# Optimization experiments

Hardware: AMD Instinct MI355X
Metric: run time of the kernel (lower is better)

Reference implementation:

```python
import jax, jax.numpy as jnp
import numpy as np

HID = 1024   # hidden_size
NH = 16      # num_heads
HD = HID // NH   # 64 head_dim
RD = int(HD * 0.25)  # 16 rotary_dim
B = 2
S = 2048
ROPE_BASE = 10000.0


def setup_inputs() -> dict:
    key = jax.random.key(0)
    ks = jax.random.split(key, 4)
    hidden_states = jax.random.normal(ks[0], (B, S, HID), jnp.float32)
    # torch nn.Linear weights: [out_features, in_features]
    Wqkv = jax.random.normal(ks[1], (3 * HID, HID), jnp.float32) * (HID ** -0.5)
    bqkv = jnp.zeros((3 * HID,), jnp.float32)
    Wd = jax.random.normal(ks[2], (HID, HID), jnp.float32) * (HID ** -0.5)
    bd = jnp.zeros((HID,), jnp.float32)
    return {"hidden_states": hidden_states, "Wqkv": Wqkv, "bqkv": bqkv, "Wd": Wd, "bd": bd}


def _rotary_tables(seq_len):
    inv_freq = 1.0 / (ROPE_BASE ** (jnp.arange(0, RD, 2, dtype=jnp.float32) / RD))
    t = jnp.arange(seq_len, dtype=jnp.float32)
    freqs = jnp.outer(t, inv_freq)                       # [S, RD/2]
    emb = jnp.concatenate([freqs, freqs], axis=-1)       # [S, RD]
    return jnp.cos(emb)[None, None], jnp.sin(emb)[None, None]  # [1,1,S,RD]


def _rotate_half(x):
    x1, x2 = jnp.split(x, 2, axis=-1)
    return jnp.concatenate([-x2, x1], axis=-1)


def reference(hidden_states, Wqkv, bqkv, Wd, bd):
    b, s, _ = hidden_states.shape
    qkv = hidden_states @ Wqkv.T + bqkv                  # [b,s,3*HID]
    qkv = qkv.reshape(b, s, 3, NH, HD).transpose(2, 0, 3, 1, 4)  # [3,b,nh,s,hd]
    q, k, v = qkv[0], qkv[1], qkv[2]

    cos, sin = _rotary_tables(s)
    q_rot, q_pass = q[..., :RD], q[..., RD:]
    k_rot, k_pass = k[..., :RD], k[..., RD:]
    q_rot = q_rot * cos + _rotate_half(q_rot) * sin
    k_rot = k_rot * cos + _rotate_half(k_rot) * sin
    q = jnp.concatenate([q_rot, q_pass], axis=-1)
    k = jnp.concatenate([k_rot, k_pass], axis=-1)

    scale = HD ** -0.5
    logits = jnp.einsum('bhqd,bhkd->bhqk', q, k) * scale  # [b,nh,s,s]
    causal_mask = jnp.triu(jnp.full((s, s), -jnp.inf, dtype=logits.dtype), 1)
    probs = jax.nn.softmax(logits + causal_mask, axis=-1)

    # KA recurrence: A_i = p_ii * V_i + sum_{j<i} p_ij * A_j
    # <=> (I - strict_lower(P)) A = diag(P) * V  -> batched triangular solve
    L = jnp.eye(s, dtype=probs.dtype) - jnp.tril(probs, -1)      # [b,nh,s,s]
    rhs = jnp.diagonal(probs, axis1=-2, axis2=-1)[..., None] * v  # [b,nh,s,hd]
    A = jax.scipy.linalg.solve_triangular(L, rhs, lower=True)     # [b,nh,s,hd]

    attn_output = A.transpose(0, 2, 1, 3).reshape(b, s, HID)
    return attn_output @ Wd.T + bd
```

## Files before the change

### kernel.cpp

```cpp
#include <hip/hip_runtime.h>
#include <math.h>

namespace {

constexpr int B  = 2, S = 2048, NH = 16, HD = 64, HID = 1024;
constexpr int BH = B * NH;
constexpr int NSTEP2 = 8;

constexpr size_t OFF_A    = 4194304;
constexpr size_t OFF_Q    = 12582912;
constexpr size_t OFF_K    = 16777216;
constexpr size_t OFF_V    = 20971520;
constexpr size_t OFF_ZI   = 25231360;
constexpr size_t OFF_PD   = 25296896;
constexpr size_t OFF_UP   = 25362432;
constexpr size_t WS_FLOATS = 29294592;

typedef __attribute__((ext_vector_type(8))) short bf16x8;
typedef __attribute__((ext_vector_type(4))) float f32x4;

__device__ inline unsigned short bf_rne(float x) {
  const unsigned u = __float_as_uint(x);
  return (unsigned short)((u + 0x7FFFu + ((u >> 16) & 1u)) >> 16);
}
__device__ inline float bf2f(short h) {
  return __uint_as_float((unsigned)(unsigned short)h << 16);
}
__device__ inline void split8(const float4 a, const float4 b,
                              bf16x8& hi, bf16x8& lo) {
  float v[8] = {a.x, a.y, a.z, a.w, b.x, b.y, b.z, b.w};
#pragma unroll
  for (int i = 0; i < 8; ++i) {
    const unsigned short h = bf_rne(v[i]);
    hi[i] = (short)h;
    lo[i] = (short)bf_rne(v[i] - bf2f((short)h));
  }
}
__device__ inline f32x4 apply3(const short* __restrict__ mh_,
                               const short* __restrict__ ml_,
                               const float* __restrict__ brow, int lg) {
  f32x4 o = (f32x4)0.f;
#pragma unroll
  for (int ks = 0; ks < 2; ++ks) {
    const bf16x8 mh = *(const bf16x8*)(mh_ + ks * 32 + lg * 8);
    const bf16x8 ml = *(const bf16x8*)(ml_ + ks * 32 + lg * 8);
    const float* bp = brow + ks * 32 + lg * 8;
    bf16x8 bh, bl;
    split8(*(const float4*)bp, *(const float4*)(bp + 4), bh, bl);
    o = __builtin_amdgcn_mfma_f32_16x16x32_bf16(mh, bh, o, 0, 0, 0);
    o = __builtin_amdgcn_mfma_f32_16x16x32_bf16(ml, bh, o, 0, 0, 0);
    o = __builtin_amdgcn_mfma_f32_16x16x32_bf16(mh, bl, o, 0, 0, 0);
  }
  return o;
}

__global__ __launch_bounds__(256) void split_pre(
    const float* __restrict__ hs, short* __restrict__ h1, short* __restrict__ l1,
    const float* __restrict__ wq, short* __restrict__ h2, short* __restrict__ l2) {
  const int n1 = B * S * HID / 4;
  const int n2 = 3 * HID * HID / 4;
  for (int g = blockIdx.x * 256 + threadIdx.x; g < n1 + n2; g += gridDim.x * 256) {
    const bool first = g < n1;
    const int idx = first ? g : g - n1;
    const float4 x = first ? *(const float4*)(hs + (size_t)idx * 4)
                           : *(const float4*)(wq + (size_t)idx * 4);
    short4 h, l;
    h.x = bf_rne(x.x); h.y = bf_rne(x.y); h.z = bf_rne(x.z); h.w = bf_rne(x.w);
    l.x = bf_rne(x.x - bf2f(h.x));
    l.y = bf_rne(x.y - bf2f(h.y));
    l.z = bf_rne(x.z - bf2f(h.z));
    l.w = bf_rne(x.w - bf2f(h.w));
    if (first) {
      *(short4*)(h1 + (size_t)idx * 4) = h;
      *(short4*)(l1 + (size_t)idx * 4) = l;
    } else {
      *(short4*)(h2 + (size_t)idx * 4) = h;
      *(short4*)(l2 + (size_t)idx * 4) = l;
    }
  }
}

__global__ __launch_bounds__(256) void split_post(
    const float* __restrict__ Abuf, short* __restrict__ h1, short* __restrict__ l1,
    const float* __restrict__ wd, short* __restrict__ h2, short* __restrict__ l2) {
  const int n1 = B * S * HID / 4;
  const int n2 = HID * HID / 4;
  for (int g = blockIdx.x * 256 + threadIdx.x; g < n1 + n2; g += gridDim.x * 256) {
    float4 x;
    if (g < n1) {
      const int m = g >> 8, q = g & 255;
      const int k0 = q * 4;
      const int b = m >> 11, s = m & (S - 1);
      const int h = k0 >> 6, d = k0 & 63;
      x = *(const float4*)(Abuf + (((size_t)(b * NH + h) * S + s) << 6) + d);
    } else {
      x = *(const float4*)(wd + (size_t)(g - n1) * 4);
    }
    short4 h, l;
    h.x = bf_rne(x.x); h.y = bf_rne(x.y); h.z = bf_rne(x.z); h.w = bf_rne(x.w);
    l.x = bf_rne(x.x - bf2f(h.x));
    l.y = bf_rne(x.y - bf2f(h.y));
    l.z = bf_rne(x.z - bf2f(h.z));
    l.w = bf_rne(x.w - bf2f(h.w));
    if (g < n1) {
      *(short4*)(h1 + (size_t)g * 4) = h;
      *(short4*)(l1 + (size_t)g * 4) = l;
    } else {
      *(short4*)(h2 + (size_t)(g - n1) * 4) = h;
      *(short4*)(l2 + (size_t)(g - n1) * 4) = l;
    }
  }
}

__global__ __launch_bounds__(256) void gemm_bf3(
    const short* __restrict__ Ahi, const short* __restrict__ Alo,
    const short* __restrict__ Bhi, const short* __restrict__ Blo,
    const float* __restrict__ bias, float* __restrict__ C,
    int M, int N, int K) {
  __shared__ short ash[128][40], als[128][40], bsh[128][40], bls[128][40];
  const int t = threadIdx.x;
  const int m0 = blockIdx.y * 128, n0 = blockIdx.x * 128;
  const int w = t >> 6, l = t & 63;
  const int wm = (w >> 1) * 64, wn = (w & 1) * 64;
  const int lr = l & 15, lk = (l >> 4) * 8;
  f32x4 acc[4][4];
#pragma unroll
  for (int i = 0; i < 4; ++i)
#pragma unroll
    for (int j = 0; j < 4; ++j) acc[i][j] = (f32x4)0.f;

  for (int kb = 0; kb < K; kb += 32) {
    __syncthreads();
#pragma unroll
    for (int i = 0; i < 2; ++i) {
      const int idx = t + i * 256;
      const int row = idx >> 2, c8 = (idx & 3) * 8;
      *(uint4*)&ash[row][c8] = *(const uint4*)(Ahi + (size_t)(m0 + row) * K + kb + c8);
      *(uint4*)&als[row][c8] = *(const uint4*)(Alo + (size_t)(m0 + row) * K + kb + c8);
      *(uint4*)&bsh[row][c8] = *(const uint4*)(Bhi + (size_t)(n0 + row) * K + kb + c8);
      *(uint4*)&bls[row][c8] = *(const uint4*)(Blo + (size_t)(n0 + row) * K + kb + c8);
    }
    __syncthreads();
    bf16x8 ah[4], al[4], bh[4], bl[4];
#pragma unroll
    for (int mi = 0; mi < 4; ++mi) {
      ah[mi] = *(const bf16x8*)&ash[wm + mi * 16 + lr][lk];
      al[mi] = *(const bf16x8*)&als[wm + mi * 16 + lr][lk];
    }
#pragma unroll
    for (int ni = 0; ni < 4; ++ni) {
      bh[ni] = *(const bf16x8*)&bsh[wn + ni * 16 + lr][lk];
      bl[ni] = *(const bf16x8*)&bls[wn + ni * 16 + lr][lk];
    }
#pragma unroll
    for (int mi = 0; mi < 4; ++mi)
#pragma unroll
      for (int ni = 0; ni < 4; ++ni) {
        acc[mi][ni] = __builtin_amdgcn_mfma_f32_16x16x32_bf16(
            ah[mi], bh[ni], acc[mi][ni], 0, 0, 0);
        acc[mi][ni] = __builtin_amdgcn_mfma_f32_16x16x32_bf16(
            al[mi], bh[ni], acc[mi][ni], 0, 0, 0);
        acc[mi][ni] = __builtin_amdgcn_mfma_f32_16x16x32_bf16(
            ah[mi], bl[ni], acc[mi][ni], 0, 0, 0);
      }
  }
  const int rq = (l >> 4) * 4;
#pragma unroll
  for (int ni = 0; ni < 4; ++ni) {
    const int col = n0 + wn + ni * 16 + lr;
    const float bv = bias[col];
#pragma unroll
    for (int mi = 0; mi < 4; ++mi)
#pragma unroll
      for (int r = 0; r < 4; ++r) {
        const int row = m0 + wm + mi * 16 + rq + r;
        C[(size_t)row * N + col] = acc[mi][ni][r] + bv;
      }
  }
}

__global__ __launch_bounds__(256) void k2_rope(
    const float* __restrict__ qkv, short* __restrict__ Qhi,
    short* __restrict__ Qlo, short* __restrict__ Khi,
    short* __restrict__ Klo, float* __restrict__ V) {
  const int g  = blockIdx.x * 256 + threadIdx.x;
  const int s  = g & (S - 1);
  const int bh = g >> 11;
  const int b  = bh >> 4, h = bh & 15;
  const float* base = qkv + ((size_t)b * S + s) * 3072 + h * 64;
  float q[64], k[64], v[64];
#pragma unroll
  for (int f = 0; f < 16; ++f) {
    const float4 x = *(const float4*)(base + f * 4);
    q[f*4+0]=x.x; q[f*4+1]=x.y; q[f*4+2]=x.z; q[f*4+3]=x.w;
    const float4 y = *(const float4*)(base + 1024 + f * 4);
    k[f*4+0]=y.x; k[f*4+1]=y.y; k[f*4+2]=y.z; k[f*4+3]=y.w;
    const float4 z = *(const float4*)(base + 2048 + f * 4);
    v[f*4+0]=z.x; v[f*4+1]=z.y; v[f*4+2]=z.z; v[f*4+3]=z.w;
  }
  const float PW[8] = {1.0f, 3.1622776601683795f, 10.0f, 31.622776601683793f,
                       100.0f, 316.22776601683796f, 1000.0f, 3162.2776601683795f};
  float qr[16], kr[16];
#pragma unroll
  for (int d = 0; d < 16; ++d) {
    const int j = d & 7;
    const float invf = 1.0f / PW[j];
    const float fr = (float)s * invf;
    float sn, c;
    sincosf(fr, &sn, &c);
    const float rq = (d < 8) ? -q[d + 8] : q[d - 8];
    const float rk = (d < 8) ? -k[d + 8] : k[d - 8];
    qr[d] = q[d] * c + rq * sn;
    kr[d] = k[d] * c + rk * sn;
  }
#pragma unroll
  for (int d = 0; d < 16; ++d) { q[d] = qr[d]; k[d] = kr[d]; }
#pragma unroll
  for (int d = 0; d < 64; ++d) q[d] *= 0.125f;
  const size_t o = ((size_t)bh * S + s) << 6;
  float* vd = V + o;
#pragma unroll
  for (int f = 0; f < 16; ++f) {
    short4 qh, ql, kh, kl;
    const float* qq = q + f * 4;
    const float* kk = k + f * 4;
    qh.x = bf_rne(qq[0]); qh.y = bf_rne(qq[1]); qh.z = bf_rne(qq[2]); qh.w = bf_rne(qq[3]);
    ql.x = bf_rne(qq[0]-bf2f(qh.x)); ql.y = bf_rne(qq[1]-bf2f(qh.y));
    ql.z = bf_rne(qq[2]-bf2f(qh.z)); ql.w = bf_rne(qq[3]-bf2f(qh.w));
    kh.x = bf_rne(kk[0]); kh.y = bf_rne(kk[1]); kh.z = bf_rne(kk[2]); kh.w = bf_rne(kk[3]);
    kl.x = bf_rne(kk[0]-bf2f(kh.x)); kl.y = bf_rne(kk[1]-bf2f(kh.y));
    kl.z = bf_rne(kk[2]-bf2f(kh.z)); kl.w = bf_rne(kk[3]-bf2f(kh.w));
    *(short4*)(Qhi + o + f*4) = qh;
    *(short4*)(Qlo + o + f*4) = ql;
    *(short4*)(Khi + o + f*4) = kh;
    *(short4*)(Klo + o + f*4) = kl;
    *(float4*)(vd + f*4) = make_float4(v[f*4], v[f*4+1], v[f*4+2], v[f*4+3]);
  }
}

__global__ __launch_bounds__(256) void k3_scores(
    const short* __restrict__ Qhi, const short* __restrict__ Qlo,
    const short* __restrict__ Khi, const short* __restrict__ Klo,
    float* __restrict__ partZ, float* __restrict__ sdg) {
  const int cb = blockIdx.x, rb = blockIdx.y, bh = blockIdx.z;
  if (cb > rb) return;
  __shared__ short qh[128][72], ql[128][72], kh[128][72], kl[128][72];
  __shared__ float red[128][2];
  const int t = threadIdx.x;
  const int w = t >> 6, l = t & 63;
  const int wm = (w >> 1) * 64, wn = (w & 1) * 64;
  const int lr = l & 15, lg = l >> 4;
  for (int v = t; v < 1024; v += 256) {
    const int r = v >> 3, c8 = (v & 7) * 8;
    const size_t gq = (((size_t)bh * S + rb * 128 + r) << 6) + c8;
    const size_t gk = (((size_t)bh * S + cb * 128 + r) << 6) + c8;
    *(uint4*)&qh[r][c8] = *(const uint4*)(Qhi + gq);
    *(uint4*)&ql[r][c8] = *(const uint4*)(Qlo + gq);
    *(uint4*)&kh[r][c8] = *(const uint4*)(Khi + gk);
    *(uint4*)&kl[r][c8] = *(const uint4*)(Klo + gk);
  }
  __syncthreads();
  f32x4 acc[4][4];
#pragma unroll
  for (int i = 0; i < 4; ++i)
#pragma unroll
    for (int j = 0; j < 4; ++j) acc[i][j] = (f32x4)0.f;
#pragma unroll
  for (int ks = 0; ks < 2; ++ks) {
    const int lk = ks * 32 + lg * 8;
    bf16x8 ah[4], al[4], bhf[4], blf[4];
#pragma unroll
    for (int mi = 0; mi < 4; ++mi) {
      ah[mi] = *(const bf16x8*)&qh[wm + mi * 16 + lr][lk];
      al[mi] = *(const bf16x8*)&ql[wm + mi * 16 + lr][lk];
    }
#pragma unroll
    for (int ni = 0; ni < 4; ++ni) {
      bhf[ni] = *(const bf16x8*)&kh[wn + ni * 16 + lr][lk];
      blf[ni] = *(const bf16x8*)&kl[wn + ni * 16 + lr][lk];
    }
#pragma unroll
    for (int mi = 0; mi < 4; ++mi)
#pragma unroll
      for (int ni = 0; ni < 4; ++ni) {
        acc[mi][ni] = __builtin_amdgcn_mfma_f32_16x16x32_bf16(
            ah[mi], bhf[ni], acc[mi][ni], 0, 0, 0);
        acc[mi][ni] = __builtin_amdgcn_mfma_f32_16x16x32_bf16(
            al[mi], bhf[ni], acc[mi][ni], 0, 0, 0);
        acc[mi][ni] = __builtin_amdgcn_mfma_f32_16x16x32_bf16(
            ah[mi], blf[ni], acc[mi][ni], 0, 0, 0);
      }
  }
  const int rq = lg * 4;
  const int rowbase = rb * 128 + wm, colbase = cb * 128 + wn;
  float rp[4][4];
#pragma unroll
  for (int mi = 0; mi < 4; ++mi)
#pragma unroll
    for (int r = 0; r < 4; ++r) rp[mi][r] = 0.f;
#pragma unroll
  for (int mi = 0; mi < 4; ++mi)
#pragma unroll
    for (int ni = 0; ni < 4; ++ni)
#pragma unroll
      for (int r = 0; r < 4; ++r) {
        const int rG = rowbase + mi * 16 + rq + r;
        const int cG = colbase + ni * 16 + lr;
        if (cG <= rG) rp[mi][r] += __expf(acc[mi][ni][r]);
        if (cG == rG) sdg[(size_t)bh * S + rG] = acc[mi][ni][r];
      }
#pragma unroll
  for (int off = 1; off < 16; off <<= 1)
#pragma unroll
    for (int mi = 0; mi < 4; ++mi)
#pragma unroll
      for (int r = 0; r < 4; ++r)
        rp[mi][r] += __shfl_xor(rp[mi][r], off, 64);
  if (lr == 0)
#pragma unroll
    for (int mi = 0; mi < 4; ++mi)
#pragma unroll
      for (int r = 0; r < 4; ++r)
        red[wm + mi * 16 + rq + r][w & 1] = rp[mi][r];
  __syncthreads();
  if (t < 128)
    partZ[(((size_t)bh * 16 + rb) * 16 + cb) * 128 + t] = red[t][0] + red[t][1];
}

__global__ __launch_bounds__(256) void k3_reduce(
    const float* __restrict__ partZ, float* __restrict__ zinv,
    float* __restrict__ pdg) {
  const int R = blockIdx.x * 256 + threadIdx.x;
  const int bh = R >> 11, r = R & 2047;
  const int rb = r >> 7, row = r & 127;
  float Z = 0.f;
  for (int c = 0; c <= rb; ++c)
    Z += partZ[(((size_t)bh*16 + rb)*16 + c)*128 + row];
  const float zi = 1.f / Z;
  zinv[R] = zi;
  pdg[R] = __expf(pdg[R]) * zi;
}

__global__ __launch_bounds__(256) void k4_minv(
    const short* __restrict__ Qhi, const short* __restrict__ Qlo,
    const short* __restrict__ Khi, const short* __restrict__ Klo,
    const float* __restrict__ zinv, short* __restrict__ Mrh,
    short* __restrict__ Mrl, short* __restrict__ P10h,
    short* __restrict__ P10l) {
  const int bh = blockIdx.y, ib = blockIdx.x;
  const int r0 = ib * 64;
  __shared__ float Nb[64][68];
  __shared__ float X[64][68];
  const int t = threadIdx.x;
  const int w = t >> 6, l = t & 63;
  const int lr = l & 15, lg = l >> 4;

  bf16x8 qfh[2], qfl[2];
  const size_t qbase = (((size_t)bh * S + r0 + 16 * w + lr) << 6);
#pragma unroll
  for (int ks = 0; ks < 2; ++ks) {
    qfh[ks] = *(const bf16x8*)(Qhi + qbase + ks * 32 + lg * 8);
    qfl[ks] = *(const bf16x8*)(Qlo + qbase + ks * 32 + lg * 8);
  }
  const int rloc0 = 16 * w + lg * 4;
  float ziv[4];
#pragma unroll
  for (int i = 0; i < 4; ++i) ziv[i] = zinv[(size_t)bh * S + r0 + rloc0 + i];

  {
    f32x4 acc[4];
#pragma unroll
    for (int i = 0; i < 4; ++i) acc[i] = (f32x4)0.f;
    const size_t kbase = ((size_t)bh * S + r0) << 6;
#pragma unroll
    for (int ks = 0; ks < 2; ++ks) {
#pragma unroll
      for (int ni = 0; ni < 4; ++ni) {
        const size_t kb = kbase + (((size_t)(16 * ni + lr)) << 6) + ks * 32 + lg * 8;
        const bf16x8 bhf = *(const bf16x8*)(Khi + kb);
        const bf16x8 blf = *(const bf16x8*)(Klo + kb);
        acc[ni] = __builtin_amdgcn_mfma_f32_16x16x32_bf16(qfh[ks], bhf, acc[ni], 0, 0, 0);
        acc[ni] = __builtin_amdgcn_mfma_f32_16x16x32_bf16(qfl[ks], bhf, acc[ni], 0, 0, 0);
        acc[ni] = __builtin_amdgcn_mfma_f32_16x16x32_bf16(qfh[ks], blf, acc[ni], 0, 0, 0);
      }
    }
#pragma unroll
    for (int ni = 0; ni < 4; ++ni) {
      const int c = 16 * ni + lr;
#pragma unroll
      for (int i = 0; i < 4; ++i) {
        const int r = rloc0 + i;
        Nb[r][c] = (c < r) ? __expf(acc[ni][i]) * ziv[i] : 0.f;
      }
    }
  }
  if (ib & 1) {
    f32x4 p[4];
#pragma unroll
    for (int i = 0; i < 4; ++i) p[i] = (f32x4)0.f;
    const size_t kbase = ((size_t)bh * S + r0 - 64) << 6;
#pragma unroll
    for (int ks = 0; ks < 2; ++ks) {
#pragma unroll
      for (int ni = 0; ni < 4; ++ni) {
        const size_t kb = kbase + (((size_t)(16 * ni + lr)) << 6) + ks * 32 + lg * 8;
        const bf16x8 bhf = *(const bf16x8*)(Khi + kb);
        const bf16x8 blf = *(const bf16x8*)(Klo + kb);
        p[ni] = __builtin_amdgcn_mfma_f32_16x16x32_bf16(qfh[ks], bhf, p[ni], 0, 0, 0);
        p[ni] = __builtin_amdgcn_mfma_f32_16x16x32_bf16(qfl[ks], bhf, p[ni], 0, 0, 0);
        p[ni] = __builtin_amdgcn_mfma_f32_16x16x32_bf16(qfh[ks], blf, p[ni], 0, 0, 0);
      }
    }
    const size_t pbase = (((size_t)bh * 16 + (ib >> 1)) * 64) * 64;
#pragma unroll
    for (int ni = 0; ni < 4; ++ni) {
      const int c = 16 * ni + lr;
#pragma unroll
      for (int i = 0; i < 4; ++i) {
        const float val = __expf(p[ni][i]) * ziv[i];
        const unsigned short h = bf_rne(val);
        P10h[pbase + (size_t)(rloc0 + i) * 64 + c] = (short)h;
        P10l[pbase + (size_t)(rloc0 + i) * 64 + c] = (short)bf_rne(val - bf2f((short)h));
      }
    }
  }
  {
    const int c = t & 63, g = t >> 6;
#pragma unroll
    for (int i = 0; i < 16; ++i) {
      const int r = 16 * g + i;
      X[r][c] = (r == c) ? 1.f : 0.f;
    }
  }
  __syncthreads();

  const int c = t & 63, g = t >> 6;
  if (w == 0) {
    for (int rr = 1; rr < 16; ++rr) {
      float a = 0.f;
      for (int j = 0; j < rr; ++j) a += Nb[rr][j] * X[j][l];
      X[rr][l] += a;
    }
  }
  __syncthreads();
#pragma unroll
  for (int I = 1; I < 4; ++I) {
    {
      const int rb4 = 16 * I + 4 * g;
      float s0 = 0.f, s1 = 0.f, s2 = 0.f, s3 = 0.f;
      for (int j = 0; j < 16 * I; j += 4) {
        const float4 n0 = *(const float4*)&Nb[rb4 + 0][j];
        const float4 n1 = *(const float4*)&Nb[rb4 + 1][j];
        const float4 n2 = *(const float4*)&Nb[rb4 + 2][j];
        const float4 n3 = *(const float4*)&Nb[rb4 + 3][j];
        const float x0 = X[j + 0][c], x1 = X[j + 1][c];
        const float x2 = X[j + 2][c], x3 = X[j + 3][c];
        s0 += n0.x * x0 + n0.y * x1 + n0.z * x2 + n0.w * x3;
        s1 += n1.x * x0 + n1.y * x1 + n1.z * x2 + n1.w * x3;
        s2 += n2.x * x0 + n2.y * x1 + n2.z * x2 + n2.w * x3;
        s3 += n3.x * x0 + n3.y * x1 + n3.z * x2 + n3.w * x3;
      }
      X[rb4 + 0][c] += s0; X[rb4 + 1][c] += s1;
      X[rb4 + 2][c] += s2; X[rb4 + 3][c] += s3;
    }
    __syncthreads();
    if (w == 0) {
      const int rb = 16 * I;
      for (int rr = 1; rr < 16; ++rr) {
        const int r = rb + rr;
        float a = 0.f;
        for (int j = rb; j < r; ++j) a += Nb[r][j] * X[j][l];
        X[r][l] += a;
      }
    }
    __syncthreads();
  }

  const size_t mb = (((size_t)bh * 32 + ib) * 64) * 64;
  for (int v = t; v < 4096; v += 256) {
    const int r = v >> 6, cc = v & 63;
    const float x = X[r][cc];
    const unsigned short h = bf_rne(x);
    Mrh[mb + v] = (short)h;
    Mrl[mb + v] = (short)bf_rne(x - bf2f((short)h));
  }
}

__global__ __launch_bounds__(256) void k5_acc(
    const short* __restrict__ Qhi, const short* __restrict__ Qlo,
    const short* __restrict__ Khi, const short* __restrict__ Klo,
    const float* __restrict__ Abuf, const float* __restrict__ zinv,
    float* __restrict__ up, int s) {
  const int bh = blockIdx.z, rh = blockIdx.y, g = blockIdx.x;
  __shared__ float Es[128][68];
  __shared__ float Ats[64][68];
  const int t = threadIdx.x;
  const int w = t >> 6, l = t & 63;
  const int lr = l & 15, lg = l >> 4;
  const int rw = 32 * w;
  const int base = s * 256 + rh * 128;

  bf16x8 qfh[2][2], qfl[2][2];
#pragma unroll
  for (int mi = 0; mi < 2; ++mi)
#pragma unroll
    for (int ks = 0; ks < 2; ++ks) {
      const size_t qo = (((size_t)bh * S + base + rw + mi * 16 + lr) << 6) + ks * 32 + lg * 8;
      qfh[mi][ks] = *(const bf16x8*)(Qhi + qo);
      qfl[mi][ks] = *(const bf16x8*)(Qlo + qo);
    }
  float ziv[2][4];
#pragma unroll
  for (int mi = 0; mi < 2; ++mi)
#pragma unroll
    for (int r = 0; r < 4; ++r)
      ziv[mi][r] = zinv[(size_t)bh * S + base + rw + mi * 16 + lg * 4 + r];

  f32x4 out[2][4];
#pragma unroll
  for (int mi = 0; mi < 2; ++mi)
#pragma unroll
    for (int ni = 0; ni < 4; ++ni) out[mi][ni] = (f32x4)0.f;

  for (int j = g; j < 2 * s; j += 7) {
    for (int h = 0; h < 2; ++h) {
      __syncthreads();
      for (int v = t; v < 1024; v += 256) {
        const int d = v & 63, sq = v >> 6;
        const size_t ab = ((size_t)bh * S + j * 128 + h * 64 + sq * 4) << 6;
        float4 o;
        o.x = Abuf[ab + d];
        o.y = Abuf[ab + 64 + d];
        o.z = Abuf[ab + 128 + d];
        o.w = Abuf[ab + 192 + d];
        *(float4*)&Ats[d][sq * 4] = o;
      }
      f32x4 qk[2][4];
#pragma unroll
      for (int mi = 0; mi < 2; ++mi)
#pragma unroll
        for (int ni = 0; ni < 4; ++ni) qk[mi][ni] = (f32x4)0.f;
#pragma unroll
      for (int ks = 0; ks < 2; ++ks) {
#pragma unroll
        for (int ni = 0; ni < 4; ++ni) {
          const size_t ko = (((size_t)bh * S + j * 128 + h * 64 + ni * 16 + lr) << 6) + ks * 32 + lg * 8;
          const bf16x8 kh8 = *(const bf16x8*)(Khi + ko);
          const bf16x8 kl8 = *(const bf16x8*)(Klo + ko);
#pragma unroll
          for (int mi = 0; mi < 2; ++mi) {
            qk[mi][ni] = __builtin_amdgcn_mfma_f32_16x16x32_bf16(
                qfh[mi][ks], kh8, qk[mi][ni], 0, 0, 0);
            qk[mi][ni] = __builtin_amdgcn_mfma_f32_16x16x32_bf16(
                qfl[mi][ks], kh8, qk[mi][ni], 0, 0, 0);
            qk[mi][ni] = __builtin_amdgcn_mfma_f32_16x16x32_bf16(
                qfh[mi][ks], kl8, qk[mi][ni], 0, 0, 0);
          }
        }
      }
#pragma unroll
      for (int mi = 0; mi < 2; ++mi)
#pragma unroll
        for (int ni = 0; ni < 4; ++ni)
#pragma unroll
          for (int r = 0; r < 4; ++r)
            Es[rw + mi * 16 + lg * 4 + r][ni * 16 + lr] =
                __expf(qk[mi][ni][r]) * ziv[mi][r];
      __syncthreads();
#pragma unroll
      for (int ks = 0; ks < 2; ++ks) {
        bf16x8 eh[2], el[2];
#pragma unroll
        for (int mi = 0; mi < 2; ++mi) {
          const float* ep = &Es[rw + mi * 16 + lr][ks * 32 + lg * 8];
          split8(*(const float4*)ep, *(const float4*)(ep + 4), eh[mi], el[mi]);
        }
#pragma unroll
        for (int ni = 0; ni < 4; ++ni) {
          const float* ap = &Ats[ni * 16 + lr][ks * 32 + lg * 8];
          bf16x8 ah8, al8;
          split8(*(const float4*)ap, *(const float4*)(ap + 4), ah8, al8);
#pragma unroll
          for (int mi = 0; mi < 2; ++mi) {
            out[mi][ni] = __builtin_amdgcn_mfma_f32_16x16x32_bf16(
                eh[mi], ah8, out[mi][ni], 0, 0, 0);
            out[mi][ni] = __builtin_amdgcn_mfma_f32_16x16x32_bf16(
                el[mi], ah8, out[mi][ni], 0, 0, 0);
            out[mi][ni] = __builtin_amdgcn_mfma_f32_16x16x32_bf16(
                eh[mi], al8, out[mi][ni], 0, 0, 0);
          }
        }
      }
    }
  }
  float* ub = up + (((size_t)(bh * 7 + g) * 2 + rh) << 13);
#pragma unroll
  for (int mi = 0; mi < 2; ++mi)
#pragma unroll
    for (int ni = 0; ni < 4; ++ni)
#pragma unroll
      for (int r = 0; r < 4; ++r)
        ub[(size_t)(rw + mi * 16 + lg * 4 + r) * 64 + ni * 16 + lr] =
            out[mi][ni][r];
}

__global__ __launch_bounds__(256) void k5_fin(
    const short* __restrict__ Qhi, const short* __restrict__ Qlo,
    const short* __restrict__ Khi, const short* __restrict__ Klo,
    const float* __restrict__ V, const float* __restrict__ pd,
    const float* __restrict__ zinv, const float* __restrict__ up,
    const short* __restrict__ Mrh, const short* __restrict__ Mrl,
    const short* __restrict__ P10h, const short* __restrict__ P10l,
    float* __restrict__ Abuf, int s) {
  const int d0 = blockIdx.x * 16;
  const int bh = blockIdx.y;
  const int t = threadIdx.x;
  const int w = t >> 6, l = t & 63;
  const int lr = l & 15, lg = l >> 4;
  const int base = s * 256;
  __shared__ float uT[16][260];
  __shared__ float aT[16][132];
  __shared__ float Es[128][68];
  const int ng = (2 * s < 7) ? 2 * s : 7;

  for (int v = t; v < 1024; v += 256) {
    const int r = v >> 2, f = v & 3;
    const int R = base + r;
    const float4 x = *(const float4*)(V + (((size_t)bh * S + R) << 6) + d0 + f * 4);
    const float p = pd[(size_t)bh * S + R];
    float a0 = p * x.x, a1 = p * x.y, a2 = p * x.z, a3 = p * x.w;
    const int rh = r >> 7, rr = r & 127;
    for (int g = 0; g < ng; ++g) {
      const float4 y = *(const float4*)(
          up + (((size_t)(bh * 7 + g) * 2 + rh) << 13) + (rr << 6) + d0 + f * 4);
      a0 += y.x; a1 += y.y; a2 += y.z; a3 += y.w;
    }
    uT[f * 4 + 0][r] = a0; uT[f * 4 + 1][r] = a1;
    uT[f * 4 + 2][r] = a2; uT[f * 4 + 3][r] = a3;
  }
  __syncthreads();
  const size_t mstep = (size_t)bh * 32 + s * 4;
  {
    const size_t mb = ((mstep + 0) * 64 + 16 * w + lr) * 64;
    const f32x4 o = apply3(Mrh + mb, Mrl + mb, &uT[lr][0], lg);
#pragma unroll
    for (int i = 0; i < 4; ++i) {
      const int r = 16 * w + lg * 4 + i;
      Abuf[(((size_t)bh * S + base + r) << 6) + d0 + lr] = o[i];
      aT[lr][r] = o[i];
    }
  }
  __syncthreads();
  {
    const size_t pb = (((size_t)bh * 16 + 2 * s) * 64 + 16 * w + lr) * 64;
    const f32x4 o = apply3(P10h + pb, P10l + pb, &aT[lr][0], lg);
#pragma unroll
    for (int i = 0; i < 4; ++i)
      uT[lr][64 + 16 * w + lg * 4 + i] += o[i];
  }
  __syncthreads();
  {
    const size_t mb = ((mstep + 1) * 64 + 16 * w + lr) * 64;
    const f32x4 o = apply3(Mrh + mb, Mrl + mb, &uT[lr][64], lg);
#pragma unroll
    for (int i = 0; i < 4; ++i) {
      const int r = 16 * w + lg * 4 + i;
      Abuf[(((size_t)bh * S + base + 64 + r) << 6) + d0 + lr] = o[i];
      aT[lr][64 + r] = o[i];
    }
  }
  {
    const int rw = 32 * w;
    bf16x8 qh_[2][2], ql_[2][2];
#pragma unroll
    for (int mi = 0; mi < 2; ++mi)
#pragma unroll
      for (int ks = 0; ks < 2; ++ks) {
        const size_t qo = (((size_t)bh * S + base + 128 + rw + mi * 16 + lr) << 6) + ks * 32 + lg * 8;
        qh_[mi][ks] = *(const bf16x8*)(Qhi + qo);
        ql_[mi][ks] = *(const bf16x8*)(Qlo + qo);
      }
    float zv[2][4];
#pragma unroll
    for (int mi = 0; mi < 2; ++mi)
#pragma unroll
      for (int i = 0; i < 4; ++i)
        zv[mi][i] = zinv[(size_t)bh * S + base + 128 + rw + mi * 16 + lg * 4 + i];
    for (int ch = 0; ch < 2; ++ch) {
      __syncthreads();
      f32x4 qk[2][4];
#pragma unroll
      for (int mi = 0; mi < 2; ++mi)
#pragma unroll
        for (int ni = 0; ni < 4; ++ni) qk[mi][ni] = (f32x4)0.f;
#pragma unroll
      for (int ks = 0; ks < 2; ++ks) {
#pragma unroll
        for (int ni = 0; ni < 4; ++ni) {
          const size_t ko = (((size_t)bh * S + base + ch * 64 + ni * 16 + lr) << 6) + ks * 32 + lg * 8;
          const bf16x8 kh8 = *(const bf16x8*)(Khi + ko);
          const bf16x8 kl8 = *(const bf16x8*)(Klo + ko);
#pragma unroll
          for (int mi = 0; mi < 2; ++mi) {
            qk[mi][ni] = __builtin_amdgcn_mfma_f32_16x16x32_bf16(
                qh_[mi][ks], kh8, qk[mi][ni], 0, 0, 0);
            qk[mi][ni] = __builtin_amdgcn_mfma_f32_16x16x32_bf16(
                ql_[mi][ks], kh8, qk[mi][ni], 0, 0, 0);
            qk[mi][ni] = __builtin_amdgcn_mfma_f32_16x16x32_bf16(
                qh_[mi][ks], kl8, qk[mi][ni], 0, 0, 0);
          }
        }
      }
#pragma unroll
      for (int mi = 0; mi < 2; ++mi)
#pragma unroll
        for (int ni = 0; ni < 4; ++ni)
#pragma unroll
          for (int i = 0; i < 4; ++i)
            Es[rw + mi * 16 + lg * 4 + i][ni * 16 + lr] =
                __expf(qk[mi][ni][i]) * zv[mi][i];
      __syncthreads();
#pragma unroll
      for (int mi = 0; mi < 2; ++mi) {
        f32x4 o = (f32x4)0.f;
#pragma unroll
        for (int kq = 0; kq < 2; ++kq) {
          const float* ep = &Es[rw + mi * 16 + lr][kq * 32 + lg * 8];
          bf16x8 eh, el;
          split8(*(const float4*)ep, *(const float4*)(ep + 4), eh, el);
          const float* ap = &aT[lr][ch * 64 + kq * 32 + lg * 8];
          bf16x8 ah, al;
          split8(*(const float4*)ap, *(const float4*)(ap + 4), ah, al);
          o = __builtin_amdgcn_mfma_f32_16x16x32_bf16(eh, ah, o, 0, 0, 0);
          o = __builtin_amdgcn_mfma_f32_16x16x32_bf16(el, ah, o, 0, 0, 0);
          o = __builtin_amdgcn_mfma_f32_16x16x32_bf16(eh, al, o, 0, 0, 0);
        }
#pragma unroll
        for (int i = 0; i < 4; ++i)
          uT[lr][128 + rw + mi * 16 + lg * 4 + i] += o[i];
      }
    }
  }
  __syncthreads();
  {
    const size_t mb = ((mstep + 2) * 64 + 16 * w + lr) * 64;
    const f32x4 o = apply3(Mrh + mb, Mrl + mb, &uT[lr][128], lg);
#pragma unroll
    for (int i = 0; i < 4; ++i) {
      const int r = 16 * w + lg * 4 + i;
      Abuf[(((size_t)bh * S + base + 128 + r) << 6) + d0 + lr] = o[i];
      aT[lr][r] = o[i];
    }
  }
  __syncthreads();
  {
    const size_t pb = (((size_t)bh * 16 + 2 * s + 1) * 64 + 16 * w + lr) * 64;
    const f32x4 o = apply3(P10h + pb, P10l + pb, &aT[lr][0], lg);
#pragma unroll
    for (int i = 0; i < 4; ++i)
      uT[lr][192 + 16 * w + lg * 4 + i] += o[i];
  }
  __syncthreads();
  {
    const size_t mb = ((mstep + 3) * 64 + 16 * w + lr) * 64;
    const f32x4 o = apply3(Mrh + mb, Mrl + mb, &uT[lr][192], lg);
#pragma unroll
    for (int i = 0; i < 4; ++i) {
      const int r = 16 * w + lg * 4 + i;
      Abuf[(((size_t)bh * S + base + 192 + r) << 6) + d0 + lr] = o[i];
    }
  }
}

}

extern "C" void kernel_launch(void* const* d_in, const int* in_sizes, int n_in,
                              void* d_out, int out_size, void* d_ws, size_t ws_size,
                              hipStream_t stream) {
  const float* hs   = (const float*)d_in[0];
  const float* Wqkv = (const float*)d_in[1];
  const float* bqkv = (const float*)d_in[2];
  const float* Wd   = (const float*)d_in[3];
  const float* bd   = (const float*)d_in[4];
  float* out = (float*)d_out;
  float* W   = (float*)d_ws;
  if (ws_size < WS_FLOATS * sizeof(float)) return;

  float* qkv   = W;
  float* partZ = W;
  float* Abuf  = W + OFF_A;
  short* Qhi   = (short*)(W + OFF_Q);
  short* Qlo   = Qhi + 4194304;
  short* Khi   = (short*)(W + OFF_K);
  short* Klo   = Khi + 4194304;
  float* Vb    = W + OFF_V;
  float* zi    = W + OFF_ZI;
  float* pdg   = W + OFF_PD;
  float* up    = W + OFF_UP;

  char* wsb = (char*)d_ws;
  short* Ahi  = (short*)(wsb + 50331648);
  short* Alo  = Ahi + 4194304;
  short* Whi  = (short*)(wsb + 67108864);
  short* Wlo  = Whi + 3145728;
  short* A2hi = (short*)(wsb + 50331648);
  short* A2lo = A2hi + 4194304;
  short* Wdhi = (short*)(wsb + 67108864);
  short* Wdlo = Wdhi + 1048576;
  short* P10h = (short*)(wsb);
  short* P10l = P10h + 2097152;
  short* Mrh  = (short*)(wsb + 33554432);
  short* Mrl  = Mrh + 4194304;

  split_pre<<<dim3(2048), 256, 0, stream>>>(hs, Ahi, Alo, Wqkv, Whi, Wlo);
  gemm_bf3<<<dim3(24, 32), 256, 0, stream>>>(Ahi, Alo, Whi, Wlo, bqkv, qkv,
                                             B*S, 3*HID, HID);
  k2_rope<<<dim3(BH * S / 256), 256, 0, stream>>>(qkv, Qhi, Qlo, Khi, Klo, Vb);
  k3_scores<<<dim3(16, 16, BH), 256, 0, stream>>>(Qhi, Qlo, Khi, Klo, partZ, pdg);
  k3_reduce<<<dim3(BH * S / 256), 256, 0, stream>>>(partZ, zi, pdg);
  k4_minv<<<dim3(S / 64, BH), 256, 0, stream>>>(Qhi, Qlo, Khi, Klo, zi,
                                                Mrh, Mrl, P10h, P10l);
  for (int s = 0; s < NSTEP2; ++s) {
    if (s > 0) {
      const int ng = (2 * s < 7) ? 2 * s : 7;
      k5_acc<<<dim3(ng, 2, BH), 256, 0, stream>>>(Qhi, Qlo, Khi, Klo, Abuf, zi,
                                                  up, s);
    }
    k5_fin<<<dim3(4, BH), 256, 0, stream>>>(Qhi, Qlo, Khi, Klo, Vb, pdg, zi, up,
                                            Mrh, Mrl, P10h, P10l, Abuf, s);
  }
  split_post<<<dim3(2048), 256, 0, stream>>>(Abuf, A2hi, A2lo, Wd, Wdhi, Wdlo);
  gemm_bf3<<<dim3(8, 32), 256, 0, stream>>>(A2hi, A2lo, Wdhi, Wdlo, bd, out,
                                            B*S, HID, HID);
}
```

Baseline: 692.5 us.

## Fuse bf16 hi/lo splitting into GEMM loads and merge k5_acc row halves

Removes the split_pre and split_post kernels: the GEMM now loads fp32 inputs and splits them into bf16 hi/lo pairs while staging into shared memory, and the output GEMM gathers directly from the per-head A buffer. This avoids writing and re-reading the split bf16 copies. Separately, k5_acc now handles both 128-row halves in one block, so each A tile loaded into shared memory is reused for twice as many query rows. The cost is halving k5_acc's grid, which raises register pressure and lowers parallelism. The GEMM also repeats the split work on every tile load.

Result: slower. 782.0 us (+12.9%).

```diff
diff --git a/kernel.cpp b/kernel.cpp
--- a/kernel.cpp
+++ b/kernel.cpp
@@ -54,67 +54,9 @@
   return o;
 }
 
-__global__ __launch_bounds__(256) void split_pre(
-    const float* __restrict__ hs, short* __restrict__ h1, short* __restrict__ l1,
-    const float* __restrict__ wq, short* __restrict__ h2, short* __restrict__ l2) {
-  const int n1 = B * S * HID / 4;
-  const int n2 = 3 * HID * HID / 4;
-  for (int g = blockIdx.x * 256 + threadIdx.x; g < n1 + n2; g += gridDim.x * 256) {
-    const bool first = g < n1;
-    const int idx = first ? g : g - n1;
-    const float4 x = first ? *(const float4*)(hs + (size_t)idx * 4)
-                           : *(const float4*)(wq + (size_t)idx * 4);
-    short4 h, l;
-    h.x = bf_rne(x.x); h.y = bf_rne(x.y); h.z = bf_rne(x.z); h.w = bf_rne(x.w);
-    l.x = bf_rne(x.x - bf2f(h.x));
-    l.y = bf_rne(x.y - bf2f(h.y));
-    l.z = bf_rne(x.z - bf2f(h.z));
-    l.w = bf_rne(x.w - bf2f(h.w));
-    if (first) {
-      *(short4*)(h1 + (size_t)idx * 4) = h;
-      *(short4*)(l1 + (size_t)idx * 4) = l;
-    } else {
-      *(short4*)(h2 + (size_t)idx * 4) = h;
-      *(short4*)(l2 + (size_t)idx * 4) = l;
-    }
-  }
-}
-
-__global__ __launch_bounds__(256) void split_post(
-    const float* __restrict__ Abuf, short* __restrict__ h1, short* __restrict__ l1,
-    const float* __restrict__ wd, short* __restrict__ h2, short* __restrict__ l2) {
-  const int n1 = B * S * HID / 4;
-  const int n2 = HID * HID / 4;
-  for (int g = blockIdx.x * 256 + threadIdx.x; g < n1 + n2; g += gridDim.x * 256) {
-    float4 x;
-    if (g < n1) {
-      const int m = g >> 8, q = g & 255;
-      const int k0 = q * 4;
-      const int b = m >> 11, s = m & (S - 1);
-      const int h = k0 >> 6, d = k0 & 63;
-      x = *(const float4*)(Abuf + (((size_t)(b * NH + h) * S + s) << 6) + d);
-    } else {
-      x = *(const float4*)(wd + (size_t)(g - n1) * 4);
-    }
-    short4 h, l;
-    h.x = bf_rne(x.x); h.y = bf_rne(x.y); h.z = bf_rne(x.z); h.w = bf_rne(x.w);
-    l.x = bf_rne(x.x - bf2f(h.x));
-    l.y = bf_rne(x.y - bf2f(h.y));
-    l.z = bf_rne(x.z - bf2f(h.z));
-    l.w = bf_rne(x.w - bf2f(h.w));
-    if (g < n1) {
-      *(short4*)(h1 + (size_t)g * 4) = h;
-      *(short4*)(l1 + (size_t)g * 4) = l;
-    } else {
-      *(short4*)(h2 + (size_t)(g - n1) * 4) = h;
-      *(short4*)(l2 + (size_t)(g - n1) * 4) = l;
-    }
-  }
-}
-
-__global__ __launch_bounds__(256) void gemm_bf3(
-    const short* __restrict__ Ahi, const short* __restrict__ Alo,
-    const short* __restrict__ Bhi, const short* __restrict__ Blo,
+template<int GATHER>
+__global__ __launch_bounds__(256) void gemm_f32(
+    const float* __restrict__ A, const float* __restrict__ Bm,
     const float* __restrict__ bias, float* __restrict__ C,
     int M, int N, int K) {
   __shared__ short ash[128][40], als[128][40], bsh[128][40], bls[128][40];
@@ -135,10 +77,24 @@
     for (int i = 0; i < 2; ++i) {
       const int idx = t + i * 256;
       const int row = idx >> 2, c8 = (idx & 3) * 8;
-      *(uint4*)&ash[row][c8] = *(const uint4*)(Ahi + (size_t)(m0 + row) * K + kb + c8);
-      *(uint4*)&als[row][c8] = *(const uint4*)(Alo + (size_t)(m0 + row) * K + kb + c8);
-      *(uint4*)&bsh[row][c8] = *(const uint4*)(Bhi + (size_t)(n0 + row) * K + kb + c8);
-      *(uint4*)&bls[row][c8] = *(const uint4*)(Blo + (size_t)(n0 + row) * K + kb + c8);
+      const float* srcA;
+      if (GATHER) {
+        const int m = m0 + row;
+        const int b = m >> 11, ss = m & (S - 1);
+        const int kk = kb + c8;
+        const int h = kk >> 6, d = kk & 63;
+        srcA = A + (((size_t)(b * NH + h) * S + ss) << 6) + d;
+      } else {
+        srcA = A + (size_t)(m0 + row) * K + kb + c8;
+      }
+      bf16x8 hi, lo;
+      split8(*(const float4*)srcA, *(const float4*)(srcA + 4), hi, lo);
+      *(bf16x8*)&ash[row][c8] = hi;
+      *(bf16x8*)&als[row][c8] = lo;
+      const float* srcB = Bm + (size_t)(n0 + row) * K + kb + c8;
+      split8(*(const float4*)srcB, *(const float4*)(srcB + 4), hi, lo);
+      *(bf16x8*)&bsh[row][c8] = hi;
+      *(bf16x8*)&bls[row][c8] = lo;
     }
     __syncthreads();
     bf16x8 ah[4], al[4], bh[4], bl[4];
@@ -491,38 +447,46 @@
     const short* __restrict__ Khi, const short* __restrict__ Klo,
     const float* __restrict__ Abuf, const float* __restrict__ zinv,
     float* __restrict__ up, int s) {
-  const int bh = blockIdx.z, rh = blockIdx.y, g = blockIdx.x;
+  const int bh = blockIdx.y, g = blockIdx.x;
   __shared__ float Es[128][68];
   __shared__ float Ats[64][68];
   const int t = threadIdx.x;
   const int w = t >> 6, l = t & 63;
   const int lr = l & 15, lg = l >> 4;
   const int rw = 32 * w;
-  const int base = s * 256 + rh * 128;
-
-  bf16x8 qfh[2][2], qfl[2][2];
-#pragma unroll
-  for (int mi = 0; mi < 2; ++mi)
-#pragma unroll
-    for (int ks = 0; ks < 2; ++ks) {
-      const size_t qo = (((size_t)bh * S + base + rw + mi * 16 + lr) << 6) + ks * 32 + lg * 8;
-      qfh[mi][ks] = *(const bf16x8*)(Qhi + qo);
-      qfl[mi][ks] = *(const bf16x8*)(Qlo + qo);
-    }
-  float ziv[2][4];
-#pragma unroll
-  for (int mi = 0; mi < 2; ++mi)
-#pragma unroll
-    for (int r = 0; r < 4; ++r)
-      ziv[mi][r] = zinv[(size_t)bh * S + base + rw + mi * 16 + lg * 4 + r];
-
-  f32x4 out[2][4];
-#pragma unroll
-  for (int mi = 0; mi < 2; ++mi)
-#pragma unroll
-    for (int ni = 0; ni < 4; ++ni) out[mi][ni] = (f32x4)0.f;
-
-  for (int j = g; j < 2 * s; j += 7) {
+  const int base = s * 256;
+
+  bf16x8 qfh[2][2][2], qfl[2][2][2];
+#pragma unroll
+  for (int rh = 0; rh < 2; ++rh)
+#pragma unroll
+    for (int mi = 0; mi < 2; ++mi)
+#pragma unroll
+      for (int ks = 0; ks < 2; ++ks) {
+        const size_t qo = (((size_t)bh * S + base + rh * 128 + rw + mi * 16 + lr) << 6)
+                          + ks * 32 + lg * 8;
+        qfh[rh][mi][ks] = *(const bf16x8*)(Qhi + qo);
+        qfl[rh][mi][ks] = *(const bf16x8*)(Qlo + qo);
+      }
+  float ziv[2][2][4];
+#pragma unroll
+  for (int rh = 0; rh < 2; ++rh)
+#pragma unroll
+    for (int mi = 0; mi < 2; ++mi)
+#pragma unroll
+      for (int r = 0; r < 4; ++r)
+        ziv[rh][mi][r] =
+            zinv[(size_t)bh * S + base + rh * 128 + rw + mi * 16 + lg * 4 + r];
+
+  f32x4 out[2][2][4];
+#pragma unroll
+  for (int rh = 0; rh < 2; ++rh)
+#pragma unroll
+    for (int mi = 0; mi < 2; ++mi)
+#pragma unroll
+      for (int ni = 0; ni < 4; ++ni) out[rh][mi][ni] = (f32x4)0.f;
+
+  for (int j = g; j < 2 * s; j += gridDim.x) {
     for (int h = 0; h < 2; ++h) {
       __syncthreads();
       for (int v = t; v < 1024; v += 256) {
@@ -535,73 +499,80 @@
         o.w = Abuf[ab + 192 + d];
         *(float4*)&Ats[d][sq * 4] = o;
       }
-      f32x4 qk[2][4];
-#pragma unroll
-      for (int mi = 0; mi < 2; ++mi)
-#pragma unroll
-        for (int ni = 0; ni < 4; ++ni) qk[mi][ni] = (f32x4)0.f;
-#pragma unroll
-      for (int ks = 0; ks < 2; ++ks) {
-#pragma unroll
-        for (int ni = 0; ni < 4; ++ni) {
-          const size_t ko = (((size_t)bh * S + j * 128 + h * 64 + ni * 16 + lr) << 6) + ks * 32 + lg * 8;
-          const bf16x8 kh8 = *(const bf16x8*)(Khi + ko);
-          const bf16x8 kl8 = *(const bf16x8*)(Klo + ko);
-#pragma unroll
-          for (int mi = 0; mi < 2; ++mi) {
-            qk[mi][ni] = __builtin_amdgcn_mfma_f32_16x16x32_bf16(
-                qfh[mi][ks], kh8, qk[mi][ni], 0, 0, 0);
-            qk[mi][ni] = __builtin_amdgcn_mfma_f32_16x16x32_bf16(
-                qfl[mi][ks], kh8, qk[mi][ni], 0, 0, 0);
-            qk[mi][ni] = __builtin_amdgcn_mfma_f32_16x16x32_bf16(
-                qfh[mi][ks], kl8, qk[mi][ni], 0, 0, 0);
+      __syncthreads();
+#pragma unroll
+      for (int rh = 0; rh < 2; ++rh) {
+        f32x4 qk[2][4];
+#pragma unroll
+        for (int mi = 0; mi < 2; ++mi)
+#pragma unroll
+          for (int ni = 0; ni < 4; ++ni) qk[mi][ni] = (f32x4)0.f;
+#pragma unroll
+        for (int ks = 0; ks < 2; ++ks) {
+#pragma unroll
+          for (int ni = 0; ni < 4; ++ni) {
+            const size_t ko = (((size_t)bh * S + j * 128 + h * 64 + ni * 16 + lr) << 6)
+                              + ks * 32 + lg * 8;
+            const bf16x8 kh8 = *(const bf16x8*)(Khi + ko);
+            const bf16x8 kl8 = *(const bf16x8*)(Klo + ko);
+#pragma unroll
+            for (int mi = 0; mi < 2; ++mi) {
+              qk[mi][ni] = __builtin_amdgcn_mfma_f32_16x16x32_bf16(
+                  qfh[rh][mi][ks], kh8, qk[mi][ni], 0, 0, 0);
+              qk[mi][ni] = __builtin_amdgcn_mfma_f32_16x16x32_bf16(
+                  qfl[rh][mi][ks], kh8, qk[mi][ni], 0, 0, 0);
+              qk[mi][ni] = __builtin_amdgcn_mfma_f32_16x16x32_bf16(
+                  qfh[rh][mi][ks], kl8, qk[mi][ni], 0, 0, 0);
+            }
           }
         }
-      }
-#pragma unroll
-      for (int mi = 0; mi < 2; ++mi)
-#pragma unroll
-        for (int ni = 0; ni < 4; ++ni)
-#pragma unroll
-          for (int r = 0; r < 4; ++r)
-            Es[rw + mi * 16 + lg * 4 + r][ni * 16 + lr] =
-                __expf(qk[mi][ni][r]) * ziv[mi][r];
-      __syncthreads();
-#pragma unroll
-      for (int ks = 0; ks < 2; ++ks) {
-        bf16x8 eh[2], el[2];
-#pragma unroll
-        for (int mi = 0; mi < 2; ++mi) {
-          const float* ep = &Es[rw + mi * 16 + lr][ks * 32 + lg * 8];
-          split8(*(const float4*)ep, *(const float4*)(ep + 4), eh[mi], el[mi]);
-        }
-#pragma unroll
-        for (int ni = 0; ni < 4; ++ni) {
-          const float* ap = &Ats[ni * 16 + lr][ks * 32 + lg * 8];
-          bf16x8 ah8, al8;
-          split8(*(const float4*)ap, *(const float4*)(ap + 4), ah8, al8);
+#pragma unroll
+        for (int mi = 0; mi < 2; ++mi)
+#pragma unroll
+          for (int ni = 0; ni < 4; ++ni)
+#pragma unroll
+            for (int r = 0; r < 4; ++r)
+              Es[rw + mi * 16 + lg * 4 + r][ni * 16 + lr] =
+                  __expf(qk[mi][ni][r]) * ziv[rh][mi][r];
+#pragma unroll
+        for (int ks = 0; ks < 2; ++ks) {
+          bf16x8 eh[2], el[2];
 #pragma unroll
           for (int mi = 0; mi < 2; ++mi) {
-            out[mi][ni] = __builtin_amdgcn_mfma_f32_16x16x32_bf16(
-                eh[mi], ah8, out[mi][ni], 0, 0, 0);
-            out[mi][ni] = __builtin_amdgcn_mfma_f32_16x16x32_bf16(
-                el[mi], ah8, out[mi][ni], 0, 0, 0);
-            out[mi][ni] = __builtin_amdgcn_mfma_f32_16x16x32_bf16(
-                eh[mi], al8, out[mi][ni], 0, 0, 0);
+            const float* ep = &Es[rw + mi * 16 + lr][ks * 32 + lg * 8];
+            split8(*(const float4*)ep, *(const float4*)(ep + 4), eh[mi], el[mi]);
+          }
+#pragma unroll
+          for (int ni = 0; ni < 4; ++ni) {
+            const float* ap = &Ats[ni * 16 + lr][ks * 32 + lg * 8];
+            bf16x8 ah8, al8;
+            split8(*(const float4*)ap, *(const float4*)(ap + 4), ah8, al8);
+#pragma unroll
+            for (int mi = 0; mi < 2; ++mi) {
+              out[rh][mi][ni] = __builtin_amdgcn_mfma_f32_16x16x32_bf16(
+                  eh[mi], ah8, out[rh][mi][ni], 0, 0, 0);
+              out[rh][mi][ni] = __builtin_amdgcn_mfma_f32_16x16x32_bf16(
+                  el[mi], ah8, out[rh][mi][ni], 0, 0, 0);
+              out[rh][mi][ni] = __builtin_amdgcn_mfma_f32_16x16x32_bf16(
+                  eh[mi], al8, out[rh][mi][ni], 0, 0, 0);
+            }
           }
         }
       }
     }
   }
-  float* ub = up + (((size_t)(bh * 7 + g) * 2 + rh) << 13);
-#pragma unroll
-  for (int mi = 0; mi < 2; ++mi)
-#pragma unroll
-    for (int ni = 0; ni < 4; ++ni)
-#pragma unroll
-      for (int r = 0; r < 4; ++r)
-        ub[(size_t)(rw + mi * 16 + lg * 4 + r) * 64 + ni * 16 + lr] =
-            out[mi][ni][r];
+#pragma unroll
+  for (int rh = 0; rh < 2; ++rh) {
+    float* ub = up + (((size_t)(bh * 7 + g) * 2 + rh) << 13);
+#pragma unroll
+    for (int mi = 0; mi < 2; ++mi)
+#pragma unroll
+      for (int ni = 0; ni < 4; ++ni)
+#pragma unroll
+        for (int r = 0; r < 4; ++r)
+          ub[(size_t)(rw + mi * 16 + lg * 4 + r) * 64 + ni * 16 + lr] =
+              out[rh][mi][ni][r];
+  }
 }
 
 __global__ __launch_bounds__(256) void k5_fin(
@@ -799,22 +770,13 @@
   float* up    = W + OFF_UP;
 
   char* wsb = (char*)d_ws;
-  short* Ahi  = (short*)(wsb + 50331648);
-  short* Alo  = Ahi + 4194304;
-  short* Whi  = (short*)(wsb + 67108864);
-  short* Wlo  = Whi + 3145728;
-  short* A2hi = (short*)(wsb + 50331648);
-  short* A2lo = A2hi + 4194304;
-  short* Wdhi = (short*)(wsb + 67108864);
-  short* Wdlo = Wdhi + 1048576;
   short* P10h = (short*)(wsb);
   short* P10l = P10h + 2097152;
   short* Mrh  = (short*)(wsb + 33554432);
   short* Mrl  = Mrh + 4194304;
 
-  split_pre<<<dim3(2048), 256, 0, stream>>>(hs, Ahi, Alo, Wqkv, Whi, Wlo);
-  gemm_bf3<<<dim3(24, 32), 256, 0, stream>>>(Ahi, Alo, Whi, Wlo, bqkv, qkv,
-                                             B*S, 3*HID, HID);
+  gemm_f32<0><<<dim3(24, 32), 256, 0, stream>>>(hs, Wqkv, bqkv, qkv,
+                                                B*S, 3*HID, HID);
   k2_rope<<<dim3(BH * S / 256), 256, 0, stream>>>(qkv, Qhi, Qlo, Khi, Klo, Vb);
   k3_scores<<<dim3(16, 16, BH), 256, 0, stream>>>(Qhi, Qlo, Khi, Klo, partZ, pdg);
   k3_reduce<<<dim3(BH * S / 256), 256, 0, stream>>>(partZ, zi, pdg);
@@ -823,13 +785,12 @@
   for (int s = 0; s < NSTEP2; ++s) {
     if (s > 0) {
       const int ng = (2 * s < 7) ? 2 * s : 7;
-      k5_acc<<<dim3(ng, 2, BH), 256, 0, stream>>>(Qhi, Qlo, Khi, Klo, Abuf, zi,
-                                                  up, s);
+      k5_acc<<<dim3(ng, BH), 256, 0, stream>>>(Qhi, Qlo, Khi, Klo, Abuf, zi,
+                                               up, s);
     }
     k5_fin<<<dim3(4, BH), 256, 0, stream>>>(Qhi, Qlo, Khi, Klo, Vb, pdg, zi, up,
                                             Mrh, Mrl, P10h, P10l, Abuf, s);
   }
-  split_post<<<dim3(2048), 256, 0, stream>>>(Abuf, A2hi, A2lo, Wd, Wdhi, Wdlo);
-  gemm_bf3<<<dim3(8, 32), 256, 0, stream>>>(A2hi, A2lo, Wdhi, Wdlo, bd, out,
-                                            B*S, HID, HID);
-}
+  gemm_f32<1><<<dim3(8, 32), 256, 0, stream>>>(Abuf, Wd, bd, out,
+                                               B*S, HID, HID);
+}
```
